# Performance work log

Measured on AMD Instinct MI355X. Metric: run time of the kernel, lower is better.

Reference implementation:

```python
import jax, jax.numpy as jnp
import numpy as np

K = 64   # target number of selected positions
R = 4    # refractory radius
B, T = 512, 32768


def setup_inputs() -> dict:
    key = jax.random.key(0)
    scores = jax.random.normal(key, (B, T), dtype=jnp.float32)
    log_temperature = jnp.zeros((), dtype=jnp.float32)  # log(init_temperature=1.0)
    return {"scores": scores, "log_temperature": log_temperature}


def reference(scores, log_temperature):
    # Differentiable soft top-K selection with refractory damping (hard=False path).
    b, t = scores.shape
    temp = jnp.clip(jnp.exp(log_temperature), 0.1, 10.0)
    y = jax.nn.sigmoid(scores / temp)                         # [B, T]
    budget = jnp.clip(jnp.sum(y, axis=1, keepdims=True), 1e-6, None)
    y = y * jnp.minimum(K / budget, 1.0)                      # scale toward budget K
    # Sequential neighbor damping over refractory radius (small fixed loop of R iters)
    for d in range(1, min(R + 1, t)):
        shift = jnp.roll(y, -d, axis=1)
        y = y * jnp.minimum(2.0 / (1.0 + y + shift), 1.0)
    return y.at[:, 0].set(0.0)
```

## Files before the change

### kernel.cpp

```cpp
#include <hip/hip_runtime.h>

#define T_LEN  32768
#define NTHR   512
#define KSEL   64.0f
#define CHUNK  16
#define HALO   10

__device__ __forceinline__ float fast_sigmoid(float x) {
    return __builtin_amdgcn_rcpf(1.0f + __expf(-x));
}

__device__ __forceinline__ float damp(float a, float b) {
    float s = a + b;
    float f = (s > 1.0f) ? 2.0f * __builtin_amdgcn_rcpf(1.0f + s) : 1.0f;
    return a * f;
}

__device__ __forceinline__ unsigned pack_bf16x2(float lo, float hi) {
    unsigned ul = __float_as_uint(lo), uh = __float_as_uint(hi);
    ul = (ul + 0x7FFFu + ((ul >> 16) & 1u)) >> 16;
    uh = (uh + 0x7FFFu + ((uh >> 16) & 1u)) >> 16;
    return ul | (uh << 16);
}

#define LDS_DWORDS (16384 + 512)

__global__ __launch_bounds__(NTHR, 4)
void selector_lds(const float* __restrict__ scores,
                  const float* __restrict__ log_temp,
                  float* __restrict__ out) {
    __shared__ unsigned ldsrow[LDS_DWORDS];
    __shared__ float red[NTHR / 64 + 1];

    const int row = blockIdx.x;
    const int tid = threadIdx.x;
    const float* srow = scores + (size_t)row * T_LEN;

    float t = expf(log_temp[0]);
    const float inv_temp = 1.0f / fminf(fmaxf(t, 0.1f), 10.0f);

    const float4* srow4 = (const float4*)srow;
    float sum = 0.0f;
    #pragma unroll
    for (int k = 0; k < 16; ++k) {
        float4 v = srow4[tid + NTHR * k];
        float s0 = fast_sigmoid(v.x * inv_temp);
        float s1 = fast_sigmoid(v.y * inv_temp);
        float s2 = fast_sigmoid(v.z * inv_temp);
        float s3 = fast_sigmoid(v.w * inv_temp);
        sum += (s0 + s1) + (s2 + s3);
        unsigned p0 = 2 * tid + 2 * NTHR * k;
        unsigned p1 = p0 + 1;
        ldsrow[p0 + (p0 >> 5)] = pack_bf16x2(s0, s1);
        ldsrow[p1 + (p1 >> 5)] = pack_bf16x2(s2, s3);
    }

    #pragma unroll
    for (int off = 32; off > 0; off >>= 1)
        sum += __shfl_down(sum, off, 64);
    const int wid = tid >> 6, lane = tid & 63;
    if (lane == 0) red[wid] = sum;
    __syncthreads();
    if (tid == 0) {
        float total = 0.0f;
        #pragma unroll
        for (int i = 0; i < NTHR / 64; ++i) total += red[i];
        red[NTHR / 64] = total;
    }
    __syncthreads();
    const float budget = fmaxf(red[NTHR / 64], 1e-6f);
    const float scale  = fminf(KSEL / budget, 1.0f);

    #pragma unroll
    for (int c = 0; c < 4; ++c) {
        const int W = CHUNK * tid + 8192 * c;
        const unsigned pbase = (unsigned)W >> 1;
        float w[CHUNK + HALO];
        #pragma unroll
        for (int j = 0; j < 13; ++j) {
            unsigned q = (pbase + j) & 16383u;
            unsigned v = ldsrow[q + (q >> 5)];
            w[2 * j]     = __uint_as_float(v << 16) * scale;
            w[2 * j + 1] = __uint_as_float(v & 0xFFFF0000u) * scale;
        }

        float m = 0.0f;
        #pragma unroll
        for (int j = 0; j < CHUNK + HALO; ++j) m = fmaxf(m, w[j]);
        if (m > 0.5f) {
            #pragma unroll
            for (int j = 0; j < 25; ++j) w[j] = damp(w[j], w[j + 1]);
            #pragma unroll
            for (int j = 0; j < 23; ++j) w[j] = damp(w[j], w[j + 2]);
            #pragma unroll
            for (int j = 0; j < 20; ++j) w[j] = damp(w[j], w[j + 3]);
            #pragma unroll
            for (int j = 0; j < 16; ++j) w[j] = damp(w[j], w[j + 4]);
        }

        if (W == 0) w[0] = 0.0f;

        float4* q4 = (float4*)(out + (size_t)row * T_LEN + W);
        q4[0] = make_float4(w[0],  w[1],  w[2],  w[3]);
        q4[1] = make_float4(w[4],  w[5],  w[6],  w[7]);
        q4[2] = make_float4(w[8],  w[9],  w[10], w[11]);
        q4[3] = make_float4(w[12], w[13], w[14], w[15]);
    }
}

extern "C" void kernel_launch(void* const* d_in, const int* in_sizes, int n_in,
                              void* d_out, int out_size, void* d_ws, size_t ws_size,
                              hipStream_t stream) {
    const float* scores = (const float*)d_in[0];
    const float* lt     = (const float*)d_in[1];
    float*       out    = (float*)d_out;
    const int B = in_sizes[0] / T_LEN;
    selector_lds<<<B, NTHR, 0, stream>>>(scores, lt, out);
}
```

Measured before the change: 121.2 us.

## Keep sigmoids in registers and skip damping via row-wide max check

Drops the bf16 LDS staging of the row. Each of 1024 threads now holds 32 sigmoid values in registers, and the block reduces the row max together with the row sum. If the scaled row max is at most 0.5, damping cannot change any value (a+b<=1 means the factor is 1), so the scaled values are stored directly with coalesced float4 writes. Otherwise the code falls back to reloading scores from global memory with halos and recomputing the sigmoid. This removes LDS traffic and bf16 rounding, at the cost of higher register pressure and a slower fallback path.

```diff
diff --git a/kernel.cpp b/kernel.cpp
--- a/kernel.cpp
+++ b/kernel.cpp
@@ -1,10 +1,8 @@
 #include <hip/hip_runtime.h>
 
 #define T_LEN  32768
-#define NTHR   512
+#define NTHR   1024
 #define KSEL   64.0f
-#define CHUNK  16
-#define HALO   10
 
 __device__ __forceinline__ float fast_sigmoid(float x) {
     return __builtin_amdgcn_rcpf(1.0f + __expf(-x));
@@ -16,78 +14,74 @@
     return a * f;
 }
 
-__device__ __forceinline__ unsigned pack_bf16x2(float lo, float hi) {
-    unsigned ul = __float_as_uint(lo), uh = __float_as_uint(hi);
-    ul = (ul + 0x7FFFu + ((ul >> 16) & 1u)) >> 16;
-    uh = (uh + 0x7FFFu + ((uh >> 16) & 1u)) >> 16;
-    return ul | (uh << 16);
-}
 
-#define LDS_DWORDS (16384 + 512)
-
-__global__ __launch_bounds__(NTHR, 4)
-void selector_lds(const float* __restrict__ scores,
-                  const float* __restrict__ log_temp,
-                  float* __restrict__ out) {
-    __shared__ unsigned ldsrow[LDS_DWORDS];
-    __shared__ float red[NTHR / 64 + 1];
-
+__global__ __launch_bounds__(NTHR, 8)
+void selector_onepass(const float* __restrict__ scores,
+                      const float* __restrict__ log_temp,
+                      float* __restrict__ out) {
     const int row = blockIdx.x;
     const int tid = threadIdx.x;
     const float* srow = scores + (size_t)row * T_LEN;
+    float*       orow = out    + (size_t)row * T_LEN;
 
     float t = expf(log_temp[0]);
     const float inv_temp = 1.0f / fminf(fmaxf(t, 0.1f), 10.0f);
 
-    const float4* srow4 = (const float4*)srow;
-    float sum = 0.0f;
+    const float4* p4 = (const float4*)srow;
+    float4 s[8];
     #pragma unroll
-    for (int k = 0; k < 16; ++k) {
-        float4 v = srow4[tid + NTHR * k];
-        float s0 = fast_sigmoid(v.x * inv_temp);
-        float s1 = fast_sigmoid(v.y * inv_temp);
-        float s2 = fast_sigmoid(v.z * inv_temp);
-        float s3 = fast_sigmoid(v.w * inv_temp);
-        sum += (s0 + s1) + (s2 + s3);
-        unsigned p0 = 2 * tid + 2 * NTHR * k;
-        unsigned p1 = p0 + 1;
-        ldsrow[p0 + (p0 >> 5)] = pack_bf16x2(s0, s1);
-        ldsrow[p1 + (p1 >> 5)] = pack_bf16x2(s2, s3);
+    for (int k = 0; k < 8; ++k) s[k] = p4[tid + NTHR * k];
+
+    float sum = 0.0f, mx = 0.0f;
+    #pragma unroll
+    for (int k = 0; k < 8; ++k) {
+        s[k].x = fast_sigmoid(s[k].x * inv_temp);
+        s[k].y = fast_sigmoid(s[k].y * inv_temp);
+        s[k].z = fast_sigmoid(s[k].z * inv_temp);
+        s[k].w = fast_sigmoid(s[k].w * inv_temp);
+        sum += (s[k].x + s[k].y) + (s[k].z + s[k].w);
+        mx = fmaxf(mx, fmaxf(fmaxf(s[k].x, s[k].y), fmaxf(s[k].z, s[k].w)));
     }
 
     #pragma unroll
-    for (int off = 32; off > 0; off >>= 1)
+    for (int off = 32; off > 0; off >>= 1) {
         sum += __shfl_down(sum, off, 64);
+        mx   = fmaxf(mx, __shfl_down(mx, off, 64));
+    }
+    __shared__ float redS[NTHR / 64 + 1];
+    __shared__ float redM[NTHR / 64 + 1];
     const int wid = tid >> 6, lane = tid & 63;
-    if (lane == 0) red[wid] = sum;
+    if (lane == 0) { redS[wid] = sum; redM[wid] = mx; }
     __syncthreads();
     if (tid == 0) {
-        float total = 0.0f;
+        float ts = 0.0f, tm = 0.0f;
         #pragma unroll
-        for (int i = 0; i < NTHR / 64; ++i) total += red[i];
-        red[NTHR / 64] = total;
+        for (int i = 0; i < NTHR / 64; ++i) { ts += redS[i]; tm = fmaxf(tm, redM[i]); }
+        redS[NTHR / 64] = ts;
+        redM[NTHR / 64] = tm;
     }
     __syncthreads();
-    const float budget = fmaxf(red[NTHR / 64], 1e-6f);
+    const float budget = fmaxf(redS[NTHR / 64], 1e-6f);
     const float scale  = fminf(KSEL / budget, 1.0f);
+    const float rowmax = redM[NTHR / 64] * scale;
 
-    #pragma unroll
-    for (int c = 0; c < 4; ++c) {
-        const int W = CHUNK * tid + 8192 * c;
-        const unsigned pbase = (unsigned)W >> 1;
-        float w[CHUNK + HALO];
+    if (rowmax <= 0.5f) {
         #pragma unroll
-        for (int j = 0; j < 13; ++j) {
-            unsigned q = (pbase + j) & 16383u;
-            unsigned v = ldsrow[q + (q >> 5)];
-            w[2 * j]     = __uint_as_float(v << 16) * scale;
-            w[2 * j + 1] = __uint_as_float(v & 0xFFFF0000u) * scale;
+        for (int k = 0; k < 8; ++k) {
+            s[k].x *= scale; s[k].y *= scale; s[k].z *= scale; s[k].w *= scale;
         }
-
-        float m = 0.0f;
+        if (tid == 0) s[0].x = 0.0f;
+        float4* q4 = (float4*)orow;
         #pragma unroll
-        for (int j = 0; j < CHUNK + HALO; ++j) m = fmaxf(m, w[j]);
-        if (m > 0.5f) {
+        for (int k = 0; k < 8; ++k) q4[tid + NTHR * k] = s[k];
+    } else {
+        #pragma unroll
+        for (int c = 0; c < 2; ++c) {
+            const int col0 = 32 * tid + 16 * c;
+            float w[26];
+            #pragma unroll
+            for (int j = 0; j < 26; ++j)
+                w[j] = fast_sigmoid(srow[(col0 + j) & (T_LEN - 1)] * inv_temp) * scale;
             #pragma unroll
             for (int j = 0; j < 25; ++j) w[j] = damp(w[j], w[j + 1]);
             #pragma unroll
@@ -96,15 +90,13 @@
             for (int j = 0; j < 20; ++j) w[j] = damp(w[j], w[j + 3]);
             #pragma unroll
             for (int j = 0; j < 16; ++j) w[j] = damp(w[j], w[j + 4]);
+            if (col0 == 0) w[0] = 0.0f;
+            float4* q4 = (float4*)(orow + col0);
+            q4[0] = make_float4(w[0],  w[1],  w[2],  w[3]);
+            q4[1] = make_float4(w[4],  w[5],  w[6],  w[7]);
+            q4[2] = make_float4(w[8],  w[9],  w[10], w[11]);
+            q4[3] = make_float4(w[12], w[13], w[14], w[15]);
         }
-
-        if (W == 0) w[0] = 0.0f;
-
-        float4* q4 = (float4*)(out + (size_t)row * T_LEN + W);
-        q4[0] = make_float4(w[0],  w[1],  w[2],  w[3]);
-        q4[1] = make_float4(w[4],  w[5],  w[6],  w[7]);
-        q4[2] = make_float4(w[8],  w[9],  w[10], w[11]);
-        q4[3] = make_float4(w[12], w[13], w[14], w[15]);
     }
 }
 
@@ -115,5 +107,5 @@
     const float* lt     = (const float*)d_in[1];
     float*       out    = (float*)d_out;
     const int B = in_sizes[0] / T_LEN;
-    selector_lds<<<B, NTHR, 0, stream>>>(scores, lt, out);
+    selector_onepass<<<B, NTHR, 0, stream>>>(scores, lt, out);
 }
```

Measured after the change: 108.6 us. 1.12x faster.
